# Optimization experiments

Hardware: AMD Instinct MI355X
Metric: run time of the kernel (lower is better)

The kernel has to match this reference:

```python
import jax, jax.numpy as jnp
import numpy as np

K = 16          # k_neighbours
BIG = 1e9       # distance penalty for masked senders


def setup_inputs() -> dict:
    key = jax.random.key(0)
    ks = jax.random.split(key, 8)
    B, N, F, H, FO = 64, 512, 64, 128, 64
    nodes = jax.random.normal(ks[0], (B, N, F), jnp.float32)
    mask = jax.random.randint(ks[1], (B, N), 0, 2, jnp.int32)

    def w(k_, sh):
        return jax.random.normal(k_, sh, jnp.float32) * (1.0 / np.sqrt(sh[0]).astype(np.float32))

    We1 = w(ks[2], (2 * F, H)); be1 = jnp.zeros((H,), jnp.float32)
    We2 = w(ks[3], (H, H));     be2 = jnp.zeros((H,), jnp.float32)
    Wn1 = w(ks[4], (F + H, H)); bn1 = jnp.zeros((H,), jnp.float32)
    Wn2 = w(ks[5], (H, FO));    bn2 = jnp.zeros((FO,), jnp.float32)
    return dict(nodes=nodes, mask=mask, We1=We1, be1=be1, We2=We2, be2=be2,
                Wn1=Wn1, bn1=bn1, Wn2=Wn2, bn2=bn2)


def reference(nodes, mask, We1, be1, We2, be2, Wn1, bn1, Wn2, bn2):
    # nodes: [B,N,F] ; mask: [B,N] (1 = real node, 0 = padding)
    m = mask.astype(nodes.dtype)                      # [B,N]
    x = nodes * m[..., None]                          # zero padded nodes

    # --- dynamic kNN graph (euclidean_squared + top_k, no self connection) ---
    sq = jnp.sum(x * x, axis=-1)                      # [B,N]
    dist = jnp.abs(sq[:, :, None] + sq[:, None, :]
                   - 2.0 * jnp.einsum('bnf,bmf->bnm', x, x))  # [B,N,N]
    dist = dist + BIG * (1.0 - m)[:, None, :]         # never select masked senders
    _, idx = jax.lax.top_k(-dist, K + 1)              # [B,N,K+1]
    idx = idx[..., 1:]                                # drop self connection -> [B,N,K]

    # --- gather sender features / masks along edges ---
    gathered = jax.vmap(lambda xf, ib: xf[ib])(x, idx)    # [B,N,K,F]
    smask = jax.vmap(lambda mv, ib: mv[ib])(m, idx)       # [B,N,K]
    recv = jnp.broadcast_to(x[:, :, None, :], gathered.shape)
    edges = jnp.concatenate([recv, gathered], axis=-1)    # [B,N,K,2F] ('concat' aggregation)

    # --- edge MLP (gather-compute) ---
    h = jax.nn.relu(edges @ We1 + be1)
    h = jax.nn.relu(h @ We2 + be2)                        # [B,N,K,H]

    # --- masked mean pooling over edges (scatter back to nodes) ---
    emask = m[:, :, None] * smask                         # edge valid iff both endpoints valid
    h = h * emask[..., None]
    cnt = jnp.maximum(jnp.sum(emask, axis=-1, keepdims=True), 1.0)  # [B,N,1]
    pooled = jnp.sum(h, axis=2) / cnt                     # [B,N,H]

    # --- node update MLP ---
    nh = jnp.concatenate([x, pooled], axis=-1)            # [B,N,F+H]
    out = jax.nn.relu(nh @ Wn1 + bn1) @ Wn2 + bn2         # [B,N,FO]
    return out * m[..., None]                             # zero padded nodes in output
```

## Files before the change

kernel.cpp:

```cpp
#include <hip/hip_runtime.h>

#define DI __device__ __forceinline__

typedef __bf16 bf16_t;
typedef __bf16 bf16x4 __attribute__((ext_vector_type(4)));
typedef __bf16 bf16x8 __attribute__((ext_vector_type(8)));
typedef float f32x4 __attribute__((ext_vector_type(4)));
typedef unsigned long long u64;


DI bf16_t f2b(float f) {
  unsigned u = __float_as_uint(f);
  unsigned r = (u + 0x7fffu + ((u >> 16) & 1u)) >> 16;
  return __builtin_bit_cast(bf16_t, (unsigned short)r);
}
DI float b2f(bf16_t h) {
  return __uint_as_float(((unsigned)__builtin_bit_cast(unsigned short, h)) << 16);
}
DI f32x4 zero4() { f32x4 z = {0.f, 0.f, 0.f, 0.f}; return z; }

DI bf16x8 make_frag(const float* p, bool wantlo) {
  float4 v0 = *(const float4*)p;
  float4 v1 = *(const float4*)(p + 4);
  float vv[8] = {v0.x, v0.y, v0.z, v0.w, v1.x, v1.y, v1.z, v1.w};
  bf16x8 a;
#pragma unroll
  for (int j = 0; j < 8; ++j) {
    bf16_t hi = f2b(vv[j]);
    a[j] = wantlo ? f2b(vv[j] - b2f(hi)) : hi;
  }
  return a;
}

DI u64 u64min(u64 a, u64 b) { return a < b ? a : b; }
template <int CTRL>
DI u64 dpp_u64(u64 v) {
  int lo = (int)(unsigned)(v & 0xffffffffull);
  int hi = (int)(unsigned)(v >> 32);
  int tlo = __builtin_amdgcn_update_dpp(0, lo, CTRL, 0xF, 0xF, true);
  int thi = __builtin_amdgcn_update_dpp(0, hi, CTRL, 0xF, 0xF, true);
  return (((u64)(unsigned)thi) << 32) | (unsigned)tlo;
}
template <int CTRL>
DI float dpp_f32(float v) {
  int t = __builtin_amdgcn_update_dpp(0, (int)__float_as_uint(v), CTRL, 0xF, 0xF, true);
  return __uint_as_float((unsigned)t);
}
DI u64 rowmin_u64(u64 v) {
  v = u64min(v, dpp_u64<0xB1>(v));
  v = u64min(v, dpp_u64<0x4E>(v));
  v = u64min(v, dpp_u64<0x141>(v));
  v = u64min(v, dpp_u64<0x140>(v));
  return v;
}
DI float rowsum_f32(float v) {
  v += dpp_f32<0xB1>(v);
  v += dpp_f32<0x4E>(v);
  v += dpp_f32<0x141>(v);
  v += dpp_f32<0x140>(v);
  return v;
}
DI void bitonic16(u64* a) {
#pragma unroll
  for (int k = 2; k <= 16; k <<= 1)
#pragma unroll
    for (int j = k >> 1; j > 0; j >>= 1)
#pragma unroll
      for (int i = 0; i < 16; ++i) {
        const int l = i ^ j;
        if (l > i) {
          const bool up = ((i & k) == 0);
          const bool sw = up ? (a[i] > a[l]) : (a[i] < a[l]);
          const u64 t0 = a[i], t1 = a[l];
          a[i] = sw ? t1 : t0;
          a[l] = sw ? t0 : t1;
        }
      }
}

__global__ void __launch_bounds__(256) kfuse(const float* __restrict__ nodes,
    const int* __restrict__ mask,
    const float* __restrict__ We1, const float* __restrict__ We2,
    const float* __restrict__ Wn1, const float* __restrict__ Wn2,
    float* __restrict__ x, bf16_t* __restrict__ xhi, bf16_t* __restrict__ xlo,
    float* __restrict__ sq, int* __restrict__ vlist, int* __restrict__ vcnt,
    bf16_t* __restrict__ W1p, bf16_t* __restrict__ W2p,
    bf16_t* __restrict__ Wn1p, bf16_t* __restrict__ Wn2p) {
  const int blk = blockIdx.x, t = threadIdx.x;
  __shared__ int cnts[8];
  __shared__ int basep[8];

  if (blk < 512) {
    const int b = blk >> 3, n0 = (blk & 7) * 64;
#pragma unroll
    for (int i = 0; i < 4; ++i) {
      const int idx = t + 256 * i;
      const int gi = b * 512 + n0 + (idx >> 4);
      const int fo = (idx & 15) * 4;
      const float fm = (float)mask[gi];
      const size_t ro = (size_t)gi * 64;
      float4 v = *(const float4*)(nodes + ro + fo);
      v.x *= fm; v.y *= fm; v.z *= fm; v.w *= fm;
      *(float4*)(x + ro + fo) = v;
      float vv[4] = {v.x, v.y, v.z, v.w};
      bf16x4 hh, ll;
#pragma unroll
      for (int k = 0; k < 4; ++k) {
        bf16_t hi = f2b(vv[k]);
        hh[k] = hi;
        ll[k] = f2b(vv[k] - b2f(hi));
      }
      *(bf16x4*)(xhi + ro + fo) = hh;
      *(bf16x4*)(xlo + ro + fo) = ll;
      float s = v.x * v.x + v.y * v.y + v.z * v.z + v.w * v.w;
      s = rowsum_f32(s);
      if ((t & 15) == 0) sq[gi] = s;
    }
  } else if (blk < 576) {
    const int b = blk - 512, lane = t & 63, w = t >> 6;
    unsigned long long bal[2]; int flag[2];
#pragma unroll
    for (int h = 0; h < 2; ++h) {
      flag[h] = (mask[b * 512 + h * 256 + t] != 0);
      bal[h] = __ballot(flag[h]);
      if (lane == 0) cnts[h * 4 + w] = __popcll(bal[h]);
    }
    __syncthreads();
    if (t == 0) {
      int a = 0;
      for (int c = 0; c < 8; ++c) { basep[c] = a; a += cnts[c]; }
      vcnt[b] = a;
    }
    __syncthreads();
#pragma unroll
    for (int h = 0; h < 2; ++h) {
      if (flag[h]) {
        const unsigned long long lt = (lane == 0) ? 0ull : (~0ull >> (64 - lane));
        const int pos = basep[h * 4 + w] + __popcll(bal[h] & lt);
        vlist[b * 512 + pos] = h * 256 + t;
      }
    }
  } else {
    int p = (blk - 576) * 256 + t;
    const float* W; bf16_t* dst; int K, Nn, local, mode;
    if (p < 4096)       { W = We1; dst = W1p;  K = 128; Nn = 128; mode = 0; local = p; }
    else if (p < 8192)  { W = We2; dst = W2p;  K = 128; Nn = 128; mode = 1; local = p - 4096; }
    else if (p < 14336) { W = Wn1; dst = Wn1p; K = 192; Nn = 128; mode = 0; local = p - 8192; }
    else                { W = Wn2; dst = Wn2p; K = 128; Nn = 64;  mode = 1; local = p - 14336; }
    int lane = local & 63;
    int nnt = (Nn >> 4);
    int chunk = local >> 6;
    int nt = chunk % nnt;
    int s = chunk / nnt;
    int n = nt * 16 + (lane & 15);
    int kbase = s * 32 + ((lane >> 4) * 8);
    bf16x8 v;
#pragma unroll
    for (int j = 0; j < 8; ++j) {
      int kp = kbase + j;
      int region = kp / K;
      int kk = kp - region * K;
      float w = W[kk * Nn + n];
      bf16_t hi = f2b(w);
      v[j] = (mode == 1 && region == 1) ? f2b(w - b2f(hi)) : hi;
    }
    *(bf16x8*)(dst + (size_t)local * 8) = v;
  }
}

__global__ void __launch_bounds__(256) kknn(const bf16_t* __restrict__ xhi,
    const bf16_t* __restrict__ xlo,
    const float* __restrict__ sq, const int* __restrict__ vlist,
    const int* __restrict__ vcnt, int* __restrict__ idxg) {
  const int b = blockIdx.x & 63, tile = blockIdx.x >> 6;
  const int nv = vcnt[b];
  if (tile * 16 >= nv) return;
  const int t = threadIdx.x, lane = t & 63, w = t >> 6;
  const int i = lane >> 4, d = lane & 15;
  __shared__ float sqs[512];
  __shared__ int vls[512];
  __shared__ __align__(16) float S[16 * 520];
  for (int k = t; k < 512; k += 256) { sqs[k] = sq[b * 512 + k]; vls[k] = vlist[b * 512 + k]; }
  __syncthreads();

  const size_t xb = (size_t)b * 512 * 64;

  const int aslot = tile * 16 + d;
  const int arow = vls[aslot < nv ? aslot : 0];
  bf16x8 ah[2], al[2];
#pragma unroll
  for (int kh = 0; kh < 2; ++kh) {
    ah[kh] = *(const bf16x8*)(xhi + xb + (size_t)arow * 64 + kh * 32 + i * 8);
    al[kh] = *(const bf16x8*)(xlo + xb + (size_t)arow * 64 + kh * 32 + i * 8);
  }

  const int rslot = tile * 16 + w * 4 + i;
  const bool vrow = (rslot < nv);
  const int nrow = vls[rslot < nv ? rslot : 0];
  const float sqn = sqs[nrow];

  int crs[8];
#pragma unroll
  for (int jj = 0; jj < 8; ++jj) {
    const int c = (w + 4 * jj) * 16 + d;
    crs[jj] = vls[c < nv ? c : 0];
  }

  bf16x8 bh[2], bl[2];
  if (w * 16 < nv) {
#pragma unroll
    for (int kh = 0; kh < 2; ++kh) {
      bh[kh] = *(const bf16x8*)(xhi + xb + (size_t)crs[0] * 64 + kh * 32 + i * 8);
      bl[kh] = *(const bf16x8*)(xlo + xb + (size_t)crs[0] * 64 + kh * 32 + i * 8);
    }
  }
  for (int jj = 0; jj < 8; ++jj) {
    const int ct = w + 4 * jj;
    if (ct * 16 >= nv) break;
    bf16x8 nbh[2], nbl[2];
    const bool pre = (jj < 7) && ((w + 4 * (jj + 1)) * 16 < nv);
    if (pre) {
#pragma unroll
      for (int kh = 0; kh < 2; ++kh) {
        nbh[kh] = *(const bf16x8*)(xhi + xb + (size_t)crs[jj + 1] * 64 + kh * 32 + i * 8);
        nbl[kh] = *(const bf16x8*)(xlo + xb + (size_t)crs[jj + 1] * 64 + kh * 32 + i * 8);
      }
    }
    f32x4 acc = zero4();
#pragma unroll
    for (int kh = 0; kh < 2; ++kh) {
      acc = __builtin_amdgcn_mfma_f32_16x16x32_bf16(ah[kh], bh[kh], acc, 0, 0, 0);
      acc = __builtin_amdgcn_mfma_f32_16x16x32_bf16(ah[kh], bl[kh], acc, 0, 0, 0);
      acc = __builtin_amdgcn_mfma_f32_16x16x32_bf16(al[kh], bh[kh], acc, 0, 0, 0);
      acc = __builtin_amdgcn_mfma_f32_16x16x32_bf16(al[kh], bl[kh], acc, 0, 0, 0);
    }
#pragma unroll
    for (int r = 0; r < 4; ++r) S[(i * 4 + r) * 520 + ct * 16 + d] = acc[r];
    if (pre) {
#pragma unroll
      for (int kh = 0; kh < 2; ++kh) { bh[kh] = nbh[kh]; bl[kh] = nbl[kh]; }
    }
  }
  __syncthreads();

  const u64 INF64 = ~0ull;
  u64 s1[16], s2[16];
#pragma unroll
  for (int j = 0; j < 16; ++j) { s1[j] = INF64; s2[j] = INF64; }
#pragma unroll
  for (int j = 0; j < 32; ++j) {
    if (j * 16 < nv) {
      const int c = j * 16 + d;
      const int m = vls[c < nv ? c : 0];
      const float dot = S[(w * 4 + i) * 520 + j * 16 + d];
      const float dd = fabsf(sqn + sqs[m] - 2.f * dot);
      const u64 key = (((u64)__float_as_uint(dd)) << 32) | (unsigned)m;
      const bool ok = (c < nv) && (m != nrow);
      if (j < 16) s1[j] = ok ? key : INF64;
      else        s2[j - 16] = ok ? key : INF64;
    }
  }
  bitonic16(s1);
  const bool two = (nv > 256);
  if (two) bitonic16(s2);

  int res = nrow;
#pragma unroll
  for (int ts = 0; ts < 16; ++ts) {
    const u64 head = two ? u64min(s1[0], s2[0]) : s1[0];
    const u64 wmin = rowmin_u64(head);
    if (d == ts) res = (wmin == INF64) ? nrow : (int)(unsigned)(wmin & 0xffffffffull);
    const bool w1 = (wmin != INF64) && (s1[0] == wmin);
#pragma unroll
    for (int k = 0; k < 15; ++k) s1[k] = w1 ? s1[k + 1] : s1[k];
    s1[15] = w1 ? INF64 : s1[15];
    if (two) {
      const bool w2 = (wmin != INF64) && (s2[0] == wmin);
#pragma unroll
      for (int k = 0; k < 15; ++k) s2[k] = w2 ? s2[k + 1] : s2[k];
      s2[15] = w2 ? INF64 : s2[15];
    }
  }
  if (vrow) idxg[((size_t)b * 512 + rslot) * 16 + d] = res;
}

__global__ void __launch_bounds__(256, 2) kedge(const bf16_t* __restrict__ xhi,
    const bf16_t* __restrict__ xlo, const int* __restrict__ idxg,
    const int* __restrict__ vlist, const int* __restrict__ vcnt,
    const bf16_t* __restrict__ W1p, const bf16_t* __restrict__ W2p,
    const float* __restrict__ be1, const float* __restrict__ be2,
    float* __restrict__ pooled) {
  __shared__ __align__(16) bf16_t wbuf[32768];
  __shared__ __align__(16) bf16_t hfrag[4][2][1024];
  const int t = threadIdx.x, lane = t & 63, w = t >> 6;
  const int q = lane >> 4, e = lane & 15;
  const int bb = blockIdx.x & 63;
  const int s0 = ((blockIdx.x >> 6) * 4 + w) * 2;

  {
    const uint4* s1 = (const uint4*)W1p;
    const uint4* s2 = (const uint4*)W2p;
    uint4* dst = (uint4*)wbuf;
#pragma unroll
    for (int i = 0; i < 8; ++i) dst[t + 256 * i] = s1[t + 256 * i];
#pragma unroll
    for (int i = 0; i < 8; ++i) dst[2048 + t + 256 * i] = s2[t + 256 * i];
  }
  __syncthreads();

  const int nv = vcnt[bb];
  if (s0 >= nv) return;

  int vl[2], sv[2];
  {
#pragma unroll
    for (int u = 0; u < 2; ++u) {
      const int sl = (s0 + u) < nv ? (s0 + u) : 0;
      vl[u] = vlist[bb * 512 + sl];
      sv[u] = idxg[((size_t)(bb * 512 + sl) << 4) + e];
    }
  }

  for (int base = s0; base < nv; base += 64) {
    const bool act1 = (base + 1) < nv;
    const int gid0 = bb * 512 + vl[0];
    const int gid1 = bb * 512 + vl[1];
    const size_t rb0 = (size_t)gid0 << 6;
    const size_t rb1 = (size_t)gid1 << 6;
    const size_t nb0 = (size_t)(bb * 512 + sv[0]) << 6;
    const size_t nb1 = (size_t)(bb * 512 + sv[1]) << 6;

    bf16x8 af[2][8];
#pragma unroll
    for (int k = 0; k < 4; ++k) {
      const int off = (k & 1) * 32 + q * 8;
      const bf16_t* pl = (k >> 1) ? xlo : xhi;
      af[0][k]     = *(const bf16x8*)(pl + rb0 + off);
      af[1][k]     = *(const bf16x8*)(pl + rb1 + off);
      af[0][4 + k] = *(const bf16x8*)(pl + nb0 + off);
      af[1][4 + k] = *(const bf16x8*)(pl + nb1 + off);
    }

    int nvl[2] = {vl[0], vl[1]}, nsv[2] = {sv[0], sv[1]};
    {
      const int nb = base + 64;
      if (nb < nv) {
#pragma unroll
        for (int u = 0; u < 2; ++u) {
          const int sl = (nb + u) < nv ? (nb + u) : 0;
          nvl[u] = vlist[bb * 512 + sl];
          nsv[u] = idxg[((size_t)(bb * 512 + sl) << 4) + e];
        }
      }
    }

    f32x4 acc[2][8];
#pragma unroll
    for (int u = 0; u < 2; ++u)
#pragma unroll
      for (int nt = 0; nt < 8; ++nt) acc[u][nt] = zero4();

#pragma unroll
    for (int ph = 0; ph < 2; ++ph)
#pragma unroll
      for (int k = 0; k < 4; ++k) {
        const bf16_t* wb = wbuf + (ph * 2 + (k & 1)) * 4096;
        const bf16x8 a0 = af[0][ph * 4 + k];
        const bf16x8 a1 = af[1][ph * 4 + k];
#pragma unroll
        for (int nt = 0; nt < 8; ++nt) {
          const bf16x8 bfv = *(const bf16x8*)(wb + (nt * 64 + lane) * 8);
          acc[0][nt] = __builtin_amdgcn_mfma_f32_16x16x32_bf16(a0, bfv, acc[0][nt], 0, 0, 0);
          acc[1][nt] = __builtin_amdgcn_mfma_f32_16x16x32_bf16(a1, bfv, acc[1][nt], 0, 0, 0);
        }
      }

    f32x4 acc2[2][8];
#pragma unroll
    for (int u = 0; u < 2; ++u)
#pragma unroll
      for (int nt = 0; nt < 8; ++nt) acc2[u][nt] = zero4();

#pragma unroll
    for (int hh = 0; hh < 2; ++hh) {
#pragma unroll
      for (int u = 0; u < 2; ++u)
#pragma unroll
        for (int nt4 = 0; nt4 < 4; ++nt4) {
          const int nt = hh * 4 + nt4;
          const int cc = nt * 16 + e;
          const float bv = be1[cc];
          const int bse = (((cc >> 5) & 1) * 64 + q * 4 + 16 * ((cc >> 3) & 3)) * 8 + (cc & 7);
#pragma unroll
          for (int r = 0; r < 4; ++r)
            hfrag[w][u][bse + r * 8] = f2b(fmaxf(acc[u][nt][r] + bv, 0.f));
        }
#pragma unroll
      for (int sl = 0; sl < 2; ++sl) {
        const int f = hh * 2 + sl;
        const bf16x8 a20 = *(const bf16x8*)(&hfrag[w][0][(sl * 64 + lane) * 8]);
        const bf16x8 a21 = *(const bf16x8*)(&hfrag[w][1][(sl * 64 + lane) * 8]);
        const bf16_t* wb2 = wbuf + 16384 + f * 4096;
#pragma unroll
        for (int nt = 0; nt < 8; ++nt) {
          const bf16x8 bfv = *(const bf16x8*)(wb2 + (nt * 64 + lane) * 8);
          acc2[0][nt] = __builtin_amdgcn_mfma_f32_16x16x32_bf16(a20, bfv, acc2[0][nt], 0, 0, 0);
          acc2[1][nt] = __builtin_amdgcn_mfma_f32_16x16x32_bf16(a21, bfv, acc2[1][nt], 0, 0, 0);
        }
      }
    }

#pragma unroll
    for (int u = 0; u < 2; ++u) {
      if (u == 0 || act1) {
        const int gid = u ? gid1 : gid0;
#pragma unroll
        for (int nt = 0; nt < 8; ++nt) {
          const float bv = be2[nt * 16 + e];
          float part = 0.f;
#pragma unroll
          for (int r = 0; r < 4; ++r) part += fmaxf(acc2[u][nt][r] + bv, 0.f);
          part += __shfl_xor(part, 16, 64);
          part += __shfl_xor(part, 32, 64);
          if (lane < 16) pooled[(size_t)gid * 128 + nt * 16 + lane] = part * 0.0625f;
        }
      }
    }

    vl[0] = nvl[0]; vl[1] = nvl[1];
    sv[0] = nsv[0]; sv[1] = nsv[1];
  }
}

__global__ void __launch_bounds__(256, 2) knode(const float* __restrict__ x,
    const float* __restrict__ pooled, const int* __restrict__ mask,
    const bf16_t* __restrict__ Wn1p, const bf16_t* __restrict__ Wn2p,
    const float* __restrict__ bn1, const float* __restrict__ bn2,
    float* __restrict__ out) {
  __shared__ __align__(16) bf16_t wbuf[32768];
  __shared__ __align__(16) bf16_t hfrag[4][1024];
  const int t = threadIdx.x, lane = t & 63, w = t >> 6;
  const int q = lane >> 4, e = lane & 15;
  const int nodebase = (blockIdx.x * 4 + w) * 16;

  {
    const uint4* s1 = (const uint4*)Wn1p;
    const uint4* s2 = (const uint4*)Wn2p;
    uint4* dst = (uint4*)wbuf;
#pragma unroll
    for (int i = 0; i < 12; ++i) dst[t + 256 * i] = s1[t + 256 * i];
#pragma unroll
    for (int i = 0; i < 4; ++i) dst[3072 + t + 256 * i] = s2[t + 256 * i];
  }
  __syncthreads();

  f32x4 acc[8];
#pragma unroll
  for (int nt = 0; nt < 8; ++nt) acc[nt] = zero4();

#pragma unroll
  for (int ph = 0; ph < 3; ++ph)
#pragma unroll
    for (int k = 0; k < 4; ++k) {
      const int s = 2 * ph + (k & 1) + (k >> 1) * 6;
      const bool wantlo = (s >= 6);
      const int sr = wantlo ? (s - 6) : s;
      const int col = sr * 32 + q * 8;
      const int node = nodebase + e;
      const float* p = (col < 64) ? (x + (size_t)node * 64 + col)
                                  : (pooled + (size_t)node * 128 + (col - 64));
      const bf16x8 af = make_frag(p, wantlo);
#pragma unroll
      for (int nt = 0; nt < 8; ++nt) {
        const bf16x8 bfv = *(const bf16x8*)(wbuf + sr * 4096 + (nt * 64 + lane) * 8);
        acc[nt] = __builtin_amdgcn_mfma_f32_16x16x32_bf16(af, bfv, acc[nt], 0, 0, 0);
      }
    }

  f32x4 acc2[4];
#pragma unroll
  for (int nt = 0; nt < 4; ++nt) acc2[nt] = zero4();

#pragma unroll
  for (int hh = 0; hh < 2; ++hh) {
#pragma unroll
    for (int nt4 = 0; nt4 < 4; ++nt4) {
      const int nt = hh * 4 + nt4;
      const int cc = nt * 16 + e;
      const float bv = bn1[cc];
      const int bse = (((cc >> 5) & 1) * 64 + q * 4 + 16 * ((cc >> 3) & 3)) * 8 + (cc & 7);
#pragma unroll
      for (int r = 0; r < 4; ++r)
        hfrag[w][bse + r * 8] = f2b(fmaxf(acc[nt][r] + bv, 0.f));
    }
#pragma unroll
    for (int sl = 0; sl < 2; ++sl) {
      const int f = hh * 2 + sl;
      const bf16x8 a2 = *(const bf16x8*)(&hfrag[w][(sl * 64 + lane) * 8]);
      const bf16_t* wb2 = wbuf + 24576 + f * 2048;
#pragma unroll
      for (int nt = 0; nt < 4; ++nt) {
        const bf16x8 bfv = *(const bf16x8*)(wb2 + (nt * 64 + lane) * 8);
        acc2[nt] = __builtin_amdgcn_mfma_f32_16x16x32_bf16(a2, bfv, acc2[nt], 0, 0, 0);
      }
    }
  }

  int mm[4];
#pragma unroll
  for (int r = 0; r < 4; ++r) mm[r] = mask[nodebase + q * 4 + r];
#pragma unroll
  for (int nt = 0; nt < 4; ++nt) {
    const float bv = bn2[nt * 16 + e];
#pragma unroll
    for (int r = 0; r < 4; ++r) {
      const int node = nodebase + q * 4 + r;
      out[(size_t)node * 64 + nt * 16 + e] = (acc2[nt][r] + bv) * (float)mm[r];
    }
  }
}

extern "C" void kernel_launch(void* const* d_in, const int* in_sizes, int n_in,
                              void* d_out, int out_size, void* d_ws, size_t ws_size,
                              hipStream_t stream) {
  const float* nodes = (const float*)d_in[0];
  const int*   mask  = (const int*)d_in[1];
  const float* We1   = (const float*)d_in[2];
  const float* be1   = (const float*)d_in[3];
  const float* We2   = (const float*)d_in[4];
  const float* be2   = (const float*)d_in[5];
  const float* Wn1   = (const float*)d_in[6];
  const float* bn1   = (const float*)d_in[7];
  const float* Wn2   = (const float*)d_in[8];
  const float* bn2   = (const float*)d_in[9];
  float* out = (float*)d_out;

  char* p = (char*)d_ws;
  auto alloc = [&](size_t bytes) -> char* {
    char* r = p;
    p += (bytes + 255) & ~(size_t)255;
    return r;
  };
  float*  x      = (float*)alloc((size_t)32768 * 64 * 4);
  bf16_t* xhi    = (bf16_t*)alloc((size_t)32768 * 64 * 2);
  bf16_t* xlo    = (bf16_t*)alloc((size_t)32768 * 64 * 2);
  float*  sq     = (float*)alloc((size_t)32768 * 4);
  int*    vlist  = (int*)alloc((size_t)32768 * 4);
  int*    vcnt   = (int*)alloc((size_t)64 * 4);
  int*    idxg   = (int*)alloc((size_t)32768 * 16 * 4);
  float*  pooled = (float*)alloc((size_t)32768 * 128 * 4);
  bf16_t* W1p    = (bf16_t*)alloc((size_t)8 * 8 * 64 * 8 * 2);
  bf16_t* W2p    = (bf16_t*)alloc((size_t)8 * 8 * 64 * 8 * 2);
  bf16_t* Wn1p   = (bf16_t*)alloc((size_t)12 * 8 * 64 * 8 * 2);
  bf16_t* Wn2p   = (bf16_t*)alloc((size_t)8 * 4 * 64 * 8 * 2);
  if ((size_t)(p - (char*)d_ws) > ws_size) return;

  kfuse<<<640, 256, 0, stream>>>(nodes, mask, We1, We2, Wn1, Wn2,
                                 x, xhi, xlo, sq, vlist, vcnt, W1p, W2p, Wn1p, Wn2p);
  kknn<<<2048, 256, 0, stream>>>(xhi, xlo, sq, vlist, vcnt, idxg);
  kedge<<<512, 256, 0, stream>>>(xhi, xlo, idxg, vlist, vcnt, W1p, W2p, be1, be2, pooled);
  knode<<<512, 256, 0, stream>>>(x, pooled, mask, Wn1p, Wn2p, bn1, bn2, out);
}
```

Measured before the change: 163.6 us.

## Use single sorted list with insertion in kNN; widen edge kernel blocks

In the kNN kernel, the second 16-entry bitonic-sorted list is replaced by sorted insertion of the remaining candidates into a single 16-entry list. This halves the register arrays and removes the dual-list merge during extraction. The edge-MLP kernel now runs 512 threads per block (8 waves) with a smaller per-wave hfrag buffer, processing the second layer in four 32-wide slices. That lowers shared memory per wave and amortizes the weight staging over more waves, in exchange for serial insertion cost when there are more than 256 valid nodes.

```diff
diff --git a/kernel.cpp b/kernel.cpp
--- a/kernel.cpp
+++ b/kernel.cpp
@@ -76,6 +76,17 @@
           a[l] = sw ? t0 : t1;
         }
       }
+}
+DI void sorted_insert16(u64* a, u64 k) {
+  u64 na[16];
+#pragma unroll
+  for (int p = 0; p < 16; ++p) {
+    const bool cur_gt = (a[p] > k);
+    const bool prv_le = (p == 0) ? true : (a[p - 1] <= k);
+    na[p] = !cur_gt ? a[p] : (prv_le ? k : a[p - 1]);
+  }
+#pragma unroll
+  for (int p = 0; p < 16; ++p) a[p] = na[p];
 }
 
 __global__ void __launch_bounds__(256) kfuse(const float* __restrict__ nodes,
@@ -244,11 +255,11 @@
   __syncthreads();
 
   const u64 INF64 = ~0ull;
-  u64 s1[16], s2[16];
-#pragma unroll
-  for (int j = 0; j < 16; ++j) { s1[j] = INF64; s2[j] = INF64; }
-#pragma unroll
-  for (int j = 0; j < 32; ++j) {
+  u64 s1[16];
+#pragma unroll
+  for (int j = 0; j < 16; ++j) s1[j] = INF64;
+#pragma unroll
+  for (int j = 0; j < 16; ++j) {
     if (j * 16 < nv) {
       const int c = j * 16 + d;
       const int m = vls[c < nv ? c : 0];
@@ -256,55 +267,54 @@
       const float dd = fabsf(sqn + sqs[m] - 2.f * dot);
       const u64 key = (((u64)__float_as_uint(dd)) << 32) | (unsigned)m;
       const bool ok = (c < nv) && (m != nrow);
-      if (j < 16) s1[j] = ok ? key : INF64;
-      else        s2[j - 16] = ok ? key : INF64;
+      s1[j] = ok ? key : INF64;
     }
   }
   bitonic16(s1);
-  const bool two = (nv > 256);
-  if (two) bitonic16(s2);
+  for (int j = 16; j * 16 < nv; ++j) {
+    const int c = j * 16 + d;
+    const int m = vls[c < nv ? c : 0];
+    const float dot = S[(w * 4 + i) * 520 + j * 16 + d];
+    const float dd = fabsf(sqn + sqs[m] - 2.f * dot);
+    const u64 key = (((u64)__float_as_uint(dd)) << 32) | (unsigned)m;
+    const bool ok = (c < nv) && (m != nrow);
+    sorted_insert16(s1, ok ? key : INF64);
+  }
 
   int res = nrow;
 #pragma unroll
   for (int ts = 0; ts < 16; ++ts) {
-    const u64 head = two ? u64min(s1[0], s2[0]) : s1[0];
-    const u64 wmin = rowmin_u64(head);
+    const u64 wmin = rowmin_u64(s1[0]);
     if (d == ts) res = (wmin == INF64) ? nrow : (int)(unsigned)(wmin & 0xffffffffull);
     const bool w1 = (wmin != INF64) && (s1[0] == wmin);
 #pragma unroll
     for (int k = 0; k < 15; ++k) s1[k] = w1 ? s1[k + 1] : s1[k];
     s1[15] = w1 ? INF64 : s1[15];
-    if (two) {
-      const bool w2 = (wmin != INF64) && (s2[0] == wmin);
-#pragma unroll
-      for (int k = 0; k < 15; ++k) s2[k] = w2 ? s2[k + 1] : s2[k];
-      s2[15] = w2 ? INF64 : s2[15];
-    }
   }
   if (vrow) idxg[((size_t)b * 512 + rslot) * 16 + d] = res;
 }
 
-__global__ void __launch_bounds__(256, 2) kedge(const bf16_t* __restrict__ xhi,
+__global__ void __launch_bounds__(512, 4) kedge(const bf16_t* __restrict__ xhi,
     const bf16_t* __restrict__ xlo, const int* __restrict__ idxg,
     const int* __restrict__ vlist, const int* __restrict__ vcnt,
     const bf16_t* __restrict__ W1p, const bf16_t* __restrict__ W2p,
     const float* __restrict__ be1, const float* __restrict__ be2,
     float* __restrict__ pooled) {
   __shared__ __align__(16) bf16_t wbuf[32768];
-  __shared__ __align__(16) bf16_t hfrag[4][2][1024];
+  __shared__ __align__(16) bf16_t hfrag[8][2][512];
   const int t = threadIdx.x, lane = t & 63, w = t >> 6;
   const int q = lane >> 4, e = lane & 15;
   const int bb = blockIdx.x & 63;
-  const int s0 = ((blockIdx.x >> 6) * 4 + w) * 2;
+  const int s0 = ((blockIdx.x >> 6) * 8 + w) * 2;
 
   {
     const uint4* s1 = (const uint4*)W1p;
     const uint4* s2 = (const uint4*)W2p;
     uint4* dst = (uint4*)wbuf;
 #pragma unroll
-    for (int i = 0; i < 8; ++i) dst[t + 256 * i] = s1[t + 256 * i];
-#pragma unroll
-    for (int i = 0; i < 8; ++i) dst[2048 + t + 256 * i] = s2[t + 256 * i];
+    for (int i = 0; i < 4; ++i) dst[t + 512 * i] = s1[t + 512 * i];
+#pragma unroll
+    for (int i = 0; i < 4; ++i) dst[2048 + t + 512 * i] = s2[t + 512 * i];
   }
   __syncthreads();
 
@@ -321,7 +331,7 @@
     }
   }
 
-  for (int base = s0; base < nv; base += 64) {
+  for (int base = s0; base < nv; base += 128) {
     const bool act1 = (base + 1) < nv;
     const int gid0 = bb * 512 + vl[0];
     const int gid1 = bb * 512 + vl[1];
@@ -343,7 +353,7 @@
 
     int nvl[2] = {vl[0], vl[1]}, nsv[2] = {sv[0], sv[1]};
     {
-      const int nb = base + 64;
+      const int nb = base + 128;
       if (nb < nv) {
 #pragma unroll
         for (int u = 0; u < 2; ++u) {
@@ -382,25 +392,23 @@
       for (int nt = 0; nt < 8; ++nt) acc2[u][nt] = zero4();
 
 #pragma unroll
-    for (int hh = 0; hh < 2; ++hh) {
+    for (int qq = 0; qq < 4; ++qq) {
 #pragma unroll
       for (int u = 0; u < 2; ++u)
 #pragma unroll
-        for (int nt4 = 0; nt4 < 4; ++nt4) {
-          const int nt = hh * 4 + nt4;
+        for (int nt2 = 0; nt2 < 2; ++nt2) {
+          const int nt = qq * 2 + nt2;
           const int cc = nt * 16 + e;
           const float bv = be1[cc];
-          const int bse = (((cc >> 5) & 1) * 64 + q * 4 + 16 * ((cc >> 3) & 3)) * 8 + (cc & 7);
+          const int bse = (q * 4 + 16 * ((cc >> 3) & 3)) * 8 + (cc & 7);
 #pragma unroll
           for (int r = 0; r < 4; ++r)
             hfrag[w][u][bse + r * 8] = f2b(fmaxf(acc[u][nt][r] + bv, 0.f));
         }
-#pragma unroll
-      for (int sl = 0; sl < 2; ++sl) {
-        const int f = hh * 2 + sl;
-        const bf16x8 a20 = *(const bf16x8*)(&hfrag[w][0][(sl * 64 + lane) * 8]);
-        const bf16x8 a21 = *(const bf16x8*)(&hfrag[w][1][(sl * 64 + lane) * 8]);
-        const bf16_t* wb2 = wbuf + 16384 + f * 4096;
+      {
+        const bf16x8 a20 = *(const bf16x8*)(&hfrag[w][0][lane * 8]);
+        const bf16x8 a21 = *(const bf16x8*)(&hfrag[w][1][lane * 8]);
+        const bf16_t* wb2 = wbuf + 16384 + qq * 4096;
 #pragma unroll
         for (int nt = 0; nt < 8; ++nt) {
           const bf16x8 bfv = *(const bf16x8*)(wb2 + (nt * 64 + lane) * 8);
@@ -558,6 +566,6 @@
   kfuse<<<640, 256, 0, stream>>>(nodes, mask, We1, We2, Wn1, Wn2,
                                  x, xhi, xlo, sq, vlist, vcnt, W1p, W2p, Wn1p, Wn2p);
   kknn<<<2048, 256, 0, stream>>>(xhi, xlo, sq, vlist, vcnt, idxg);
-  kedge<<<512, 256, 0, stream>>>(xhi, xlo, idxg, vlist, vcnt, W1p, W2p, be1, be2, pooled);
+  kedge<<<512, 512, 0, stream>>>(xhi, xlo, idxg, vlist, vcnt, W1p, W2p, be1, be2, pooled);
   knode<<<512, 256, 0, stream>>>(x, pooled, mask, Wn1p, Wn2p, bn1, bn2, out);
 }
```

Result: slower. 241.3 us (+47.5%).
